# Kernel tuning notes

Measured on AMD Instinct MI355X. Metric: run time of the kernel, lower is better.

The kernel has to match this reference:

```python
import jax, jax.numpy as jnp
import numpy as np

B, T, D, H = 4, 2048, 1024, 16
DK = D // H  # 64
EPS = 1e-5


def _rope(q, k, offset=0):
    # q, k: (B, H, T, DK). Standard rotate-half RoPE, base 10000.
    half = DK // 2
    inv_freq = 1.0 / (10000.0 ** (jnp.arange(0, half, dtype=jnp.float32) / half))
    pos = jnp.arange(q.shape[2], dtype=jnp.float32) + offset  # (T,)
    freqs = pos[:, None] * inv_freq[None, :]          # (T, half)
    cos = jnp.concatenate([jnp.cos(freqs)] * 2, -1)   # (T, DK)
    sin = jnp.concatenate([jnp.sin(freqs)] * 2, -1)

    def rot(x):
        x1, x2 = x[..., :half], x[..., half:]
        return jnp.concatenate([-x2, x1], axis=-1)

    q = q * cos + rot(q) * sin
    k = k * cos + rot(k) * sin
    return q, k


def setup_inputs() -> dict:
    key = jax.random.key(0)
    k0, k1, k2 = jax.random.split(key, 3)
    s = 0.02
    return {
        "x": jax.random.normal(k0, (B, T, D), jnp.float32),
        "ln_w": jnp.ones((D,), jnp.float32),
        "ln_b": jnp.zeros((D,), jnp.float32),
        "w_qkv": jax.random.normal(k1, (D, 3 * D), jnp.float32) * s,
        "b_qkv": jnp.zeros((3 * D,), jnp.float32),
        "w_o": jax.random.normal(k2, (D, D), jnp.float32) * s,
        "b_o": jnp.zeros((D,), jnp.float32),
    }


def reference(x, ln_w, ln_b, w_qkv, b_qkv, w_o, b_o):
    # LayerNorm
    mu = jnp.mean(x, axis=-1, keepdims=True)
    var = jnp.mean(jnp.square(x - mu), axis=-1, keepdims=True)
    h = (x - mu) * jax.lax.rsqrt(var + EPS) * ln_w + ln_b

    # Fused QKV projection -> (B, T, 3, H, DK) -> per-head (B, H, T, DK)
    qkv = (h @ w_qkv + b_qkv).reshape(B, T, 3, H, DK)
    q = qkv[:, :, 0].transpose(0, 2, 1, 3)
    k = qkv[:, :, 1].transpose(0, 2, 1, 3)
    v = qkv[:, :, 2].transpose(0, 2, 1, 3)

    q, k = _rope(q, k, offset=0)

    # Causal SDPA
    scale = 1.0 / np.sqrt(DK)
    scores = jnp.einsum("bhqd,bhkd->bhqk", q, k) * scale
    causal = jnp.tril(jnp.ones((T, T), dtype=bool))
    scores = jnp.where(causal, scores, jnp.finfo(scores.dtype).min)
    attn = jax.nn.softmax(scores, axis=-1)
    out = jnp.einsum("bhqk,bhkd->bhqd", attn, v)

    out = out.transpose(0, 2, 1, 3).reshape(B, T, D)
    return out @ w_o + b_o
```

## Files before the change

kernel.cpp:

```cpp
#include <hip/hip_runtime.h>
#include <math.h>

#define B_ 4
#define T_ 2048
#define D_ 1024
#define H_ 16
#define DK_ 64
#define EPS_ 1e-5f

typedef __attribute__((ext_vector_type(4))) float f32x4;
typedef __attribute__((ext_vector_type(8))) short sv8;
typedef __attribute__((ext_vector_type(4))) short sv4;

__device__ __forceinline__ short f2bf(float f) {
  union { float f; unsigned u; } x; x.f = f;
  unsigned r = x.u + 0x7fffu + ((x.u >> 16) & 1u);
  return (short)(r >> 16);
}

__global__ __launch_bounds__(256) void rope_tab(float2* __restrict__ cs) {
  const int i = blockIdx.x * 256 + threadIdx.x;
  const int t = i >> 5, f = i & 31;
  const float inv = powf(10000.0f, -(float)f / 32.0f);
  float sn, cn;
  sincosf((float)t * inv, &sn, &cn);
  cs[i] = make_float2(cn, sn);
}

__global__ __launch_bounds__(256) void ln_kernel(const float* __restrict__ x,
                                                 const float* __restrict__ w,
                                                 const float* __restrict__ b,
                                                 short* __restrict__ h) {
  const int row = blockIdx.x;
  const float4 v = ((const float4*)(x + (size_t)row * D_))[threadIdx.x];
  float s  = v.x + v.y + v.z + v.w;
  float ss = v.x*v.x + v.y*v.y + v.z*v.z + v.w*v.w;
  #pragma unroll
  for (int o = 32; o > 0; o >>= 1) {
    s  += __shfl_down(s,  o);
    ss += __shfl_down(ss, o);
  }
  __shared__ float red[8];
  const int wid = threadIdx.x >> 6, lane = threadIdx.x & 63;
  if (lane == 0) { red[wid] = s; red[wid + 4] = ss; }
  __syncthreads();
  s  = red[0] + red[1] + red[2] + red[3];
  ss = red[4] + red[5] + red[6] + red[7];
  const float mu  = s * (1.0f / D_);
  const float var = ss * (1.0f / D_) - mu * mu;
  const float inv = rsqrtf(var + EPS_);
  const float4 wv = ((const float4*)w)[threadIdx.x];
  const float4 bv = ((const float4*)b)[threadIdx.x];
  sv4 o;
  o[0] = f2bf((v.x - mu) * inv * wv.x + bv.x);
  o[1] = f2bf((v.y - mu) * inv * wv.y + bv.y);
  o[2] = f2bf((v.z - mu) * inv * wv.z + bv.z);
  o[3] = f2bf((v.w - mu) * inv * wv.w + bv.w);
  ((sv4*)(h + (size_t)row * D_))[threadIdx.x] = o;
}

__global__ __launch_bounds__(256) void conv_t(const float* __restrict__ W,
                                              short* __restrict__ WT,
                                              int K, int N) {
  __shared__ float tile[32][33];
  const int k0 = blockIdx.y * 32, n0 = blockIdx.x * 32;
  const int tx = threadIdx.x & 31, ty = threadIdx.x >> 5;
  #pragma unroll
  for (int i = 0; i < 4; ++i) {
    const int k = ty * 4 + i;
    tile[k][tx] = W[(size_t)(k0 + k) * N + n0 + tx];
  }
  __syncthreads();
  #pragma unroll
  for (int i = 0; i < 4; ++i) {
    const int n = ty * 4 + i;
    WT[(size_t)(n0 + n) * K + k0 + tx] = f2bf(tile[tx][n]);
  }
}

#define GBM 128
#define GBN 128
#define GBK 32

__global__ __launch_bounds__(256) void gemm_qkv_rope(const short* __restrict__ A,
                                                     const short* __restrict__ BT,
                                                     const float* __restrict__ bias,
                                                     const float2* __restrict__ cs,
                                                     short* __restrict__ qb,
                                                     short* __restrict__ kb,
                                                     short* __restrict__ vt) {
  __shared__ __align__(16) short As[GBM][GBK];
  __shared__ __align__(16) short Bs[GBN][GBK];
  const int tid = threadIdx.x;
  const int l = tid & 63, g = l >> 4, lq = l & 15;
  const int wm = (tid >> 6) >> 1, wn = (tid >> 6) & 1;
  const int m0 = blockIdx.y * GBM, n0 = blockIdx.x * GBN;
  const int M = B_ * T_, N = 3 * D_, K = D_;
  (void)M;

  f32x4 acc[4][4] = {};

  for (int k0 = 0; k0 < K; k0 += GBK) {
    __syncthreads();
    #pragma unroll
    for (int r = 0; r < 2; ++r) {
      const int c = tid + r * 256;
      const int row = c >> 2, co = (c & 3) * 8;
      *(int4*)&As[row][co] = *(const int4*)(A + (size_t)(m0 + row) * K + k0 + co);
      *(int4*)&Bs[row][co] = *(const int4*)(BT + (size_t)(n0 + row) * K + k0 + co);
    }
    __syncthreads();
    sv8 af[4], bf[4];
    #pragma unroll
    for (int mi = 0; mi < 4; ++mi) af[mi] = *(const sv8*)&As[64 * wm + 16 * mi + lq][8 * g];
    #pragma unroll
    for (int ni = 0; ni < 4; ++ni) bf[ni] = *(const sv8*)&Bs[64 * wn + 16 * ni + lq][8 * g];
    #pragma unroll
    for (int mi = 0; mi < 4; ++mi)
      #pragma unroll
      for (int ni = 0; ni < 4; ++ni)
        acc[mi][ni] = __builtin_amdgcn_mfma_f32_16x16x32_bf16(af[mi], bf[ni], acc[mi][ni], 0, 0, 0);
  }

  const int sec = n0 >> 10;
  if (sec < 2) {
    short* dst = (sec == 0) ? qb : kb;
    const float qs = (sec == 0) ? 0.125f : 1.0f;
    #pragma unroll
    for (int nA = 0; nA < 2; ++nA) {
      const int colA = n0 + 64 * wn + 16 * nA + lq;
      const float bA = bias[colA], bB = bias[colA + 32];
      const int clA = colA & 1023;
      const int f = 16 * nA + lq;
      #pragma unroll
      for (int mi = 0; mi < 4; ++mi) {
        const int rbase = m0 + 64 * wm + 16 * mi + 4 * g;
        #pragma unroll
        for (int r = 0; r < 4; ++r) {
          const int row = rbase + r, t = row & (T_ - 1);
          const float2 c_s = cs[t * 32 + f];
          const float x1 = acc[mi][nA][r] + bA;
          const float x2 = acc[mi][nA + 2][r] + bB;
          dst[(size_t)row * D_ + clA]      = f2bf((x1 * c_s.x - x2 * c_s.y) * qs);
          dst[(size_t)row * D_ + clA + 32] = f2bf((x2 * c_s.x + x1 * c_s.y) * qs);
        }
      }
    }
  } else {
    #pragma unroll
    for (int ni = 0; ni < 4; ++ni) {
      const int col = n0 + 64 * wn + 16 * ni + lq;
      const float bb = bias[col];
      const int cl = col & 1023;
      const int hh = cl >> 6, d = cl & 63;
      #pragma unroll
      for (int mi = 0; mi < 4; ++mi) {
        const int rbase = m0 + 64 * wm + 16 * mi + 4 * g;
        #pragma unroll
        for (int r = 0; r < 4; ++r) {
          const int row = rbase + r;
          const int bI = row >> 11, t = row & (T_ - 1);
          vt[((size_t)(bI * H_ + hh) * DK_ + d) * T_ + t] = f2bf(acc[mi][ni][r] + bb);
        }
      }
    }
  }
}

__global__ __launch_bounds__(256) void gemm_bf16(const short* __restrict__ A,
                                                 const short* __restrict__ BT,
                                                 const float* __restrict__ bias,
                                                 float* __restrict__ C,
                                                 int M, int N, int K) {
  __shared__ __align__(16) short As[GBM][GBK];
  __shared__ __align__(16) short Bs[GBN][GBK];
  const int tid = threadIdx.x;
  const int l = tid & 63, g = l >> 4, lq = l & 15;
  const int wm = (tid >> 6) >> 1, wn = (tid >> 6) & 1;
  const int m0 = blockIdx.y * GBM, n0 = blockIdx.x * GBN;

  f32x4 acc[4][4] = {};

  for (int k0 = 0; k0 < K; k0 += GBK) {
    __syncthreads();
    #pragma unroll
    for (int r = 0; r < 2; ++r) {
      const int c = tid + r * 256;
      const int row = c >> 2, co = (c & 3) * 8;
      *(int4*)&As[row][co] = *(const int4*)(A + (size_t)(m0 + row) * K + k0 + co);
      *(int4*)&Bs[row][co] = *(const int4*)(BT + (size_t)(n0 + row) * K + k0 + co);
    }
    __syncthreads();
    sv8 af[4], bf[4];
    #pragma unroll
    for (int mi = 0; mi < 4; ++mi) af[mi] = *(const sv8*)&As[64 * wm + 16 * mi + lq][8 * g];
    #pragma unroll
    for (int ni = 0; ni < 4; ++ni) bf[ni] = *(const sv8*)&Bs[64 * wn + 16 * ni + lq][8 * g];
    #pragma unroll
    for (int mi = 0; mi < 4; ++mi)
      #pragma unroll
      for (int ni = 0; ni < 4; ++ni)
        acc[mi][ni] = __builtin_amdgcn_mfma_f32_16x16x32_bf16(af[mi], bf[ni], acc[mi][ni], 0, 0, 0);
  }

  #pragma unroll
  for (int ni = 0; ni < 4; ++ni) {
    const int col = n0 + 64 * wn + 16 * ni + lq;
    const float bb = bias[col];
    #pragma unroll
    for (int mi = 0; mi < 4; ++mi) {
      const int rbase = m0 + 64 * wm + 16 * mi + 4 * g;
      #pragma unroll
      for (int r = 0; r < 4; ++r)
        C[(size_t)(rbase + r) * N + col] = acc[mi][ni][r] + bb;
    }
  }
}

__global__ __launch_bounds__(256) void flash_mfma(const short* __restrict__ qb,
                                                  const short* __restrict__ kb,
                                                  const short* __restrict__ vt,
                                                  short* __restrict__ out) {
  __shared__ __align__(16) short Ks[64][72];
  __shared__ __align__(16) short Vt[64][72];
  __shared__ __align__(16) short Ps[4][16][72];

  const int tid = threadIdx.x;
  const int w = tid >> 6, l = tid & 63, g = l >> 4, lq = l & 15;
  const int bx = blockIdx.x, hh = blockIdx.y, b = blockIdx.z;
  const int q0 = bx * 64;

  const int qrow = q0 + 16 * w + lq;
  const short* qp = qb + (size_t)(b * T_ + qrow) * D_ + hh * DK_;
  sv8 qf[2];
  qf[0] = *(const sv8*)(qp + 8 * g);
  qf[1] = *(const sv8*)(qp + 32 + 8 * g);

  f32x4 o[4] = {{0,0,0,0},{0,0,0,0},{0,0,0,0},{0,0,0,0}};
  float m_run = -INFINITY, l_run = 0.0f;

  const short* kbB = kb + (size_t)(b * T_) * D_ + hh * DK_;
  const short* vtB = vt + (size_t)(b * H_ + hh) * DK_ * T_;

  const int niter = bx + 1;
  const int skey = tid >> 3, sj = tid & 7;

  int4 kr0, kr1, vr0, vr1;
  {
    kr0 = *(const int4*)(kbB + (size_t)(skey)      * D_ + sj * 8);
    kr1 = *(const int4*)(kbB + (size_t)(skey + 32) * D_ + sj * 8);
    vr0 = *(const int4*)(vtB + (size_t)(skey)      * T_ + sj * 8);
    vr1 = *(const int4*)(vtB + (size_t)(skey + 32) * T_ + sj * 8);
  }

  for (int it = 0; it < niter; ++it) {
    const int kv0 = it * 64;
    __syncthreads();
    *(int4*)&Ks[skey][sj * 8]      = kr0;
    *(int4*)&Ks[skey + 32][sj * 8] = kr1;
    *(int4*)&Vt[skey][sj * 8]      = vr0;
    *(int4*)&Vt[skey + 32][sj * 8] = vr1;
    __syncthreads();

    if (it + 1 < niter) {
      const int nk = kv0 + 64;
      kr0 = *(const int4*)(kbB + (size_t)(nk + skey)      * D_ + sj * 8);
      kr1 = *(const int4*)(kbB + (size_t)(nk + skey + 32) * D_ + sj * 8);
      vr0 = *(const int4*)(vtB + (size_t)(skey)      * T_ + nk + sj * 8);
      vr1 = *(const int4*)(vtB + (size_t)(skey + 32) * T_ + nk + sj * 8);
    }

    float sv[4][4];
    #pragma unroll
    for (int kt = 0; kt < 4; ++kt) {
      f32x4 acc = {0, 0, 0, 0};
      #pragma unroll
      for (int s = 0; s < 2; ++s) {
        const sv8 kf = *(const sv8*)&Ks[kt * 16 + lq][32 * s + 8 * g];
        acc = __builtin_amdgcn_mfma_f32_16x16x32_bf16(kf, qf[s], acc, 0, 0, 0);
      }
      sv[kt][0] = acc[0]; sv[kt][1] = acc[1]; sv[kt][2] = acc[2]; sv[kt][3] = acc[3];
    }

    if (it == niter - 1) {
      #pragma unroll
      for (int kt = 0; kt < 4; ++kt)
        #pragma unroll
        for (int r = 0; r < 4; ++r) {
          const int key_abs = kv0 + kt * 16 + 4 * g + r;
          if (key_abs > qrow) sv[kt][r] = -INFINITY;
        }
    }

    float tm = -INFINITY;
    #pragma unroll
    for (int kt = 0; kt < 4; ++kt)
      #pragma unroll
      for (int r = 0; r < 4; ++r) tm = fmaxf(tm, sv[kt][r]);
    tm = fmaxf(tm, __shfl_xor(tm, 16));
    tm = fmaxf(tm, __shfl_xor(tm, 32));
    const float mn = fmaxf(m_run, tm);
    const float alpha = __expf(m_run - mn);
    float psum = 0.0f;
    #pragma unroll
    for (int kt = 0; kt < 4; ++kt)
      #pragma unroll
      for (int r = 0; r < 4; ++r) {
        const float p = __expf(sv[kt][r] - mn);
        sv[kt][r] = p;
        psum += p;
      }
    psum += __shfl_xor(psum, 16);
    psum += __shfl_xor(psum, 32);
    l_run = l_run * alpha + psum;
    m_run = mn;

    #pragma unroll
    for (int r = 0; r < 4; ++r) {
      const float ar = __shfl(alpha, 4 * g + r);
      o[0][r] *= ar; o[1][r] *= ar; o[2][r] *= ar; o[3][r] *= ar;
    }

    #pragma unroll
    for (int kt = 0; kt < 4; ++kt) {
      sv4 p4;
      p4[0] = f2bf(sv[kt][0]); p4[1] = f2bf(sv[kt][1]);
      p4[2] = f2bf(sv[kt][2]); p4[3] = f2bf(sv[kt][3]);
      *(sv4*)&Ps[w][lq][kt * 16 + 4 * g] = p4;
    }

    #pragma unroll
    for (int s = 0; s < 2; ++s) {
      const sv8 pa = *(const sv8*)&Ps[w][lq][32 * s + 8 * g];
      #pragma unroll
      for (int dt = 0; dt < 4; ++dt) {
        const sv8 vb = *(const sv8*)&Vt[dt * 16 + lq][32 * s + 8 * g];
        o[dt] = __builtin_amdgcn_mfma_f32_16x16x32_bf16(pa, vb, o[dt], 0, 0, 0);
      }
    }
  }

  #pragma unroll
  for (int r = 0; r < 4; ++r) {
    const float li = __shfl(l_run, 4 * g + r);
    const float inv = 1.0f / li;
    const int qr = q0 + 16 * w + 4 * g + r;
    short* op = out + (size_t)(b * T_ + qr) * D_ + hh * DK_;
    #pragma unroll
    for (int dt = 0; dt < 4; ++dt)
      op[dt * 16 + lq] = f2bf(o[dt][r] * inv);
  }
}

extern "C" void kernel_launch(void* const* d_in, const int* in_sizes, int n_in,
                              void* d_out, int out_size, void* d_ws, size_t ws_size,
                              hipStream_t stream) {
  const float* x     = (const float*)d_in[0];
  const float* ln_w  = (const float*)d_in[1];
  const float* ln_b  = (const float*)d_in[2];
  const float* w_qkv = (const float*)d_in[3];
  const float* b_qkv = (const float*)d_in[4];
  const float* w_o   = (const float*)d_in[5];
  const float* b_o   = (const float*)d_in[6];
  float* outp = (float*)d_out;

  const int rows = B_ * T_;
  const size_t nHD = (size_t)rows * D_;

  short* h      = (short*)d_ws;
  short* qb     = h + nHD;
  short* kb     = qb + nHD;
  short* vt     = kb + nHD;
  short* att    = vt + nHD;
  short* wqkvT  = att + nHD;
  short* woT    = wqkvT + (size_t)D_ * 3 * D_;
  float2* csT   = (float2*)(woT + (size_t)D_ * D_);

  rope_tab<<<T_ * 32 / 256, 256, 0, stream>>>(csT);
  conv_t<<<dim3(3 * D_ / 32, D_ / 32), 256, 0, stream>>>(w_qkv, wqkvT, D_, 3 * D_);
  conv_t<<<dim3(D_ / 32, D_ / 32), 256, 0, stream>>>(w_o, woT, D_, D_);

  ln_kernel<<<rows, 256, 0, stream>>>(x, ln_w, ln_b, h);

  {
    dim3 grid(3 * D_ / GBN, rows / GBM);
    gemm_qkv_rope<<<grid, 256, 0, stream>>>(h, wqkvT, b_qkv, csT, qb, kb, vt);
  }

  {
    dim3 grid(T_ / 64, H_, B_);
    flash_mfma<<<grid, 256, 0, stream>>>(qb, kb, vt, att);
  }

  {
    dim3 grid(D_ / GBN, rows / GBM);
    gemm_bf16<<<grid, 256, 0, stream>>>(att, woT, b_o, outp, rows, D_, D_);
  }
}
```

Baseline: 374.1 us.

## Double-buffer GEMMs with direct LDS loads and streamline flash softmax

Both GEMMs now stage A/B tiles straight into double-buffered LDS with global_load_lds, prefetching the next K-slice while MFMAs run on the current one. The flash kernel folds log2(e) into the Q scale so it can use exp2, skips rescaling the output unless the row max grows by more than 8, converts probabilities to bf16 with a packed cvt instruction, and linearizes the grid so consecutive blocks share the same query tile index. These target global load latency, exp cost and rescale overhead in attention. Risks: one barrier per iteration with async LDS writes may race without an explicit vmcnt wait, and the lazy max-update can slightly change numerics.

```diff
diff --git a/kernel.cpp b/kernel.cpp
--- a/kernel.cpp
+++ b/kernel.cpp
@@ -7,6 +7,7 @@
 #define H_ 16
 #define DK_ 64
 #define EPS_ 1e-5f
+#define LOG2E 1.44269504f
 
 typedef __attribute__((ext_vector_type(4))) float f32x4;
 typedef __attribute__((ext_vector_type(8))) short sv8;
@@ -16,6 +17,11 @@
   union { float f; unsigned u; } x; x.f = f;
   unsigned r = x.u + 0x7fffu + ((x.u >> 16) & 1u);
   return (short)(r >> 16);
+}
+
+__device__ __forceinline__ void gload16(const void* g, void* l) {
+  __builtin_amdgcn_global_load_lds((const __attribute__((address_space(1))) void*)g,
+                                   (__attribute__((address_space(3))) void*)l, 16, 0, 0);
 }
 
 __global__ __launch_bounds__(256) void rope_tab(float2* __restrict__ cs) {
@@ -82,6 +88,19 @@
 #define GBN 128
 #define GBK 32
 
+__device__ __forceinline__ void gstage(const short* __restrict__ A,
+                                       const short* __restrict__ BT,
+                                       short* AsB, short* BsB,
+                                       int tid, size_t aoff, size_t boff) {
+  #pragma unroll
+  for (int rr = 0; rr < 2; ++rr) {
+    const int c = tid + rr * 256;
+    const int row = c >> 2, co = (c & 3) * 8;
+    gload16(A + aoff + (size_t)row * D_ + co, AsB + c * 8);
+    gload16(BT + boff + (size_t)row * D_ + co, BsB + c * 8);
+  }
+}
+
 __global__ __launch_bounds__(256) void gemm_qkv_rope(const short* __restrict__ A,
                                                      const short* __restrict__ BT,
                                                      const float* __restrict__ bias,
@@ -89,43 +108,39 @@
                                                      short* __restrict__ qb,
                                                      short* __restrict__ kb,
                                                      short* __restrict__ vt) {
-  __shared__ __align__(16) short As[GBM][GBK];
-  __shared__ __align__(16) short Bs[GBN][GBK];
+  __shared__ __align__(16) short As[2][GBM][GBK];
+  __shared__ __align__(16) short Bs[2][GBN][GBK];
   const int tid = threadIdx.x;
   const int l = tid & 63, g = l >> 4, lq = l & 15;
   const int wm = (tid >> 6) >> 1, wn = (tid >> 6) & 1;
   const int m0 = blockIdx.y * GBM, n0 = blockIdx.x * GBN;
-  const int M = B_ * T_, N = 3 * D_, K = D_;
-  (void)M;
 
   f32x4 acc[4][4] = {};
 
-  for (int k0 = 0; k0 < K; k0 += GBK) {
+  gstage(A, BT, &As[0][0][0], &Bs[0][0][0], tid, (size_t)m0 * D_, (size_t)n0 * D_);
+  int cur = 0;
+  for (int k0 = 0; k0 < D_; k0 += GBK) {
     __syncthreads();
-    #pragma unroll
-    for (int r = 0; r < 2; ++r) {
-      const int c = tid + r * 256;
-      const int row = c >> 2, co = (c & 3) * 8;
-      *(int4*)&As[row][co] = *(const int4*)(A + (size_t)(m0 + row) * K + k0 + co);
-      *(int4*)&Bs[row][co] = *(const int4*)(BT + (size_t)(n0 + row) * K + k0 + co);
-    }
-    __syncthreads();
+    if (k0 + GBK < D_)
+      gstage(A, BT, &As[cur ^ 1][0][0], &Bs[cur ^ 1][0][0], tid,
+             (size_t)m0 * D_ + k0 + GBK, (size_t)n0 * D_ + k0 + GBK);
     sv8 af[4], bf[4];
     #pragma unroll
-    for (int mi = 0; mi < 4; ++mi) af[mi] = *(const sv8*)&As[64 * wm + 16 * mi + lq][8 * g];
-    #pragma unroll
-    for (int ni = 0; ni < 4; ++ni) bf[ni] = *(const sv8*)&Bs[64 * wn + 16 * ni + lq][8 * g];
+    for (int mi = 0; mi < 4; ++mi) af[mi] = *(const sv8*)&As[cur][64 * wm + 16 * mi + lq][8 * g];
+    #pragma unroll
+    for (int ni = 0; ni < 4; ++ni) bf[ni] = *(const sv8*)&Bs[cur][64 * wn + 16 * ni + lq][8 * g];
     #pragma unroll
     for (int mi = 0; mi < 4; ++mi)
       #pragma unroll
       for (int ni = 0; ni < 4; ++ni)
         acc[mi][ni] = __builtin_amdgcn_mfma_f32_16x16x32_bf16(af[mi], bf[ni], acc[mi][ni], 0, 0, 0);
+    cur ^= 1;
   }
 
   const int sec = n0 >> 10;
   if (sec < 2) {
     short* dst = (sec == 0) ? qb : kb;
-    const float qs = (sec == 0) ? 0.125f : 1.0f;
+    const float qs = (sec == 0) ? 0.125f * LOG2E : 1.0f;
     #pragma unroll
     for (int nA = 0; nA < 2; ++nA) {
       const int colA = n0 + 64 * wn + 16 * nA + lq;
@@ -171,9 +186,9 @@
                                                  const short* __restrict__ BT,
                                                  const float* __restrict__ bias,
                                                  float* __restrict__ C,
-                                                 int M, int N, int K) {
-  __shared__ __align__(16) short As[GBM][GBK];
-  __shared__ __align__(16) short Bs[GBN][GBK];
+                                                 int M, int N) {
+  __shared__ __align__(16) short As[2][GBM][GBK];
+  __shared__ __align__(16) short Bs[2][GBN][GBK];
   const int tid = threadIdx.x;
   const int l = tid & 63, g = l >> 4, lq = l & 15;
   const int wm = (tid >> 6) >> 1, wn = (tid >> 6) & 1;
@@ -181,26 +196,24 @@
 
   f32x4 acc[4][4] = {};
 
-  for (int k0 = 0; k0 < K; k0 += GBK) {
+  gstage(A, BT, &As[0][0][0], &Bs[0][0][0], tid, (size_t)m0 * D_, (size_t)n0 * D_);
+  int cur = 0;
+  for (int k0 = 0; k0 < D_; k0 += GBK) {
     __syncthreads();
-    #pragma unroll
-    for (int r = 0; r < 2; ++r) {
-      const int c = tid + r * 256;
-      const int row = c >> 2, co = (c & 3) * 8;
-      *(int4*)&As[row][co] = *(const int4*)(A + (size_t)(m0 + row) * K + k0 + co);
-      *(int4*)&Bs[row][co] = *(const int4*)(BT + (size_t)(n0 + row) * K + k0 + co);
-    }
-    __syncthreads();
+    if (k0 + GBK < D_)
+      gstage(A, BT, &As[cur ^ 1][0][0], &Bs[cur ^ 1][0][0], tid,
+             (size_t)m0 * D_ + k0 + GBK, (size_t)n0 * D_ + k0 + GBK);
     sv8 af[4], bf[4];
     #pragma unroll
-    for (int mi = 0; mi < 4; ++mi) af[mi] = *(const sv8*)&As[64 * wm + 16 * mi + lq][8 * g];
-    #pragma unroll
-    for (int ni = 0; ni < 4; ++ni) bf[ni] = *(const sv8*)&Bs[64 * wn + 16 * ni + lq][8 * g];
+    for (int mi = 0; mi < 4; ++mi) af[mi] = *(const sv8*)&As[cur][64 * wm + 16 * mi + lq][8 * g];
+    #pragma unroll
+    for (int ni = 0; ni < 4; ++ni) bf[ni] = *(const sv8*)&Bs[cur][64 * wn + 16 * ni + lq][8 * g];
     #pragma unroll
     for (int mi = 0; mi < 4; ++mi)
       #pragma unroll
       for (int ni = 0; ni < 4; ++ni)
         acc[mi][ni] = __builtin_amdgcn_mfma_f32_16x16x32_bf16(af[mi], bf[ni], acc[mi][ni], 0, 0, 0);
+    cur ^= 1;
   }
 
   #pragma unroll
@@ -227,10 +240,12 @@
 
   const int tid = threadIdx.x;
   const int w = tid >> 6, l = tid & 63, g = l >> 4, lq = l & 15;
-  const int bx = blockIdx.x, hh = blockIdx.y, b = blockIdx.z;
+  const int wg = blockIdx.x;
+  const int pair = wg & 63, bx = wg >> 6;
+  const int hh = pair & 15, b = pair >> 4;
   const int q0 = bx * 64;
-
   const int qrow = q0 + 16 * w + lq;
+
   const short* qp = qb + (size_t)(b * T_ + qrow) * D_ + hh * DK_;
   sv8 qf[2];
   qf[0] = *(const sv8*)(qp + 8 * g);
@@ -241,8 +256,8 @@
 
   const short* kbB = kb + (size_t)(b * T_) * D_ + hh * DK_;
   const short* vtB = vt + (size_t)(b * H_ + hh) * DK_ * T_;
-
   const int niter = bx + 1;
+
   const int skey = tid >> 3, sj = tid & 7;
 
   int4 kr0, kr1, vr0, vr1;
@@ -299,34 +314,37 @@
       for (int r = 0; r < 4; ++r) tm = fmaxf(tm, sv[kt][r]);
     tm = fmaxf(tm, __shfl_xor(tm, 16));
     tm = fmaxf(tm, __shfl_xor(tm, 32));
-    const float mn = fmaxf(m_run, tm);
-    const float alpha = __expf(m_run - mn);
+    if (__any(tm > m_run + 8.0f)) {
+      const float mn = fmaxf(m_run, tm);
+      const float alpha = __builtin_amdgcn_exp2f(m_run - mn);
+      l_run *= alpha;
+      #pragma unroll
+      for (int r = 0; r < 4; ++r) {
+        const float ar = __shfl(alpha, 4 * g + r);
+        o[0][r] *= ar; o[1][r] *= ar; o[2][r] *= ar; o[3][r] *= ar;
+      }
+      m_run = mn;
+    }
     float psum = 0.0f;
     #pragma unroll
     for (int kt = 0; kt < 4; ++kt)
       #pragma unroll
       for (int r = 0; r < 4; ++r) {
-        const float p = __expf(sv[kt][r] - mn);
+        const float p = __builtin_amdgcn_exp2f(sv[kt][r] - m_run);
         sv[kt][r] = p;
         psum += p;
       }
     psum += __shfl_xor(psum, 16);
     psum += __shfl_xor(psum, 32);
-    l_run = l_run * alpha + psum;
-    m_run = mn;
-
-    #pragma unroll
-    for (int r = 0; r < 4; ++r) {
-      const float ar = __shfl(alpha, 4 * g + r);
-      o[0][r] *= ar; o[1][r] *= ar; o[2][r] *= ar; o[3][r] *= ar;
-    }
+    l_run += psum;
 
     #pragma unroll
     for (int kt = 0; kt < 4; ++kt) {
-      sv4 p4;
-      p4[0] = f2bf(sv[kt][0]); p4[1] = f2bf(sv[kt][1]);
-      p4[2] = f2bf(sv[kt][2]); p4[3] = f2bf(sv[kt][3]);
-      *(sv4*)&Ps[w][lq][kt * 16 + 4 * g] = p4;
+      unsigned pa_, pb_;
+      asm("v_cvt_pk_bf16_f32 %0, %1, %2" : "=v"(pa_) : "v"(sv[kt][0]), "v"(sv[kt][1]));
+      asm("v_cvt_pk_bf16_f32 %0, %1, %2" : "=v"(pb_) : "v"(sv[kt][2]), "v"(sv[kt][3]));
+      int2 pk; pk.x = (int)pa_; pk.y = (int)pb_;
+      *(int2*)&Ps[w][lq][kt * 16 + 4 * g] = pk;
     }
 
     #pragma unroll
@@ -388,12 +406,11 @@
   }
 
   {
-    dim3 grid(T_ / 64, H_, B_);
-    flash_mfma<<<grid, 256, 0, stream>>>(qb, kb, vt, att);
+    flash_mfma<<<(T_ / 64) * H_ * B_, 256, 0, stream>>>(qb, kb, vt, att);
   }
 
   {
     dim3 grid(D_ / GBN, rows / GBM);
-    gemm_bf16<<<grid, 256, 0, stream>>>(att, woT, b_o, outp, rows, D_, D_);
-  }
-}
+    gemm_bf16<<<grid, 256, 0, stream>>>(att, woT, b_o, outp, rows, D_);
+  }
+}
```

Result: faster. 305.3 us (-18.4%).
